# Optimization experiments

Measured on AMD Instinct MI355X. Metric: run time of the kernel, lower is better.

## Reference

```python
import jax, jax.numpy as jnp
import numpy as np

TAU_M = 20.0
DT = 1.0
V_TH = 1.0
V_RESET = 0.0
ALPHA = float(np.exp(-DT / TAU_M))  # membrane decay per step

B, T, I, H, O = 64, 1024, 128, 512, 10


def spike_fn(v):
    # Heaviside spike; surrogate grad handled in fwdbwd module.
    return (v >= 0.0).astype(v.dtype)


def setup_inputs() -> dict:
    key = jax.random.key(0)
    k = jax.random.split(key, 6)
    x = jax.random.normal(k[0], (B, T, I), dtype=jnp.float32)
    # input_projection: Linear(I, H) -> weight [H, I], bias [H]
    Wi = jax.random.normal(k[1], (H, I), dtype=jnp.float32) * (1.0 / np.sqrt(I))
    bi = jnp.zeros((H,), dtype=jnp.float32)
    # recurrent weight [H, H] (xavier-ish)
    Wr = jax.random.normal(k[2], (H, H), dtype=jnp.float32) * float(np.sqrt(2.0 / (H + H)))
    # readout: Linear(H, O)
    Wo = jax.random.normal(k[3], (O, H), dtype=jnp.float32) * (1.0 / np.sqrt(H))
    bo = jnp.zeros((O,), dtype=jnp.float32)
    return {"x": x, "Wi": Wi, "bi": bi, "Wr": Wr, "Wo": Wo, "bo": bo}


def reference(x, Wi, bi, Wr, Wo, bo):
    # Precompute input projection for all timesteps: [B, T, H]
    x_proj = jnp.einsum('bti,hi->bth', x, Wi) + bi

    def step(carry, cur_t):
        h, spikes_prev = carry
        total_current = cur_t + spikes_prev @ Wr        # [B, H]
        h = ALPHA * h + total_current                    # LIF leak + integrate
        spikes = spike_fn(h - V_TH)                      # threshold
        h = spikes * V_RESET + (1.0 - spikes) * h        # reset on spike
        return (h, spikes), spikes

    h0 = jnp.zeros((x.shape[0], Wr.shape[0]), dtype=x.dtype)
    s0 = jnp.zeros_like(h0)
    (_, _), hidden_states = jax.lax.scan(step, (h0, s0), jnp.swapaxes(x_proj, 0, 1))
    hidden_states = jnp.swapaxes(hidden_states, 0, 1)    # [B, T, H]

    hidden_mean = hidden_states.mean(axis=1)             # rate readout
    output = hidden_mean @ Wo.T + bo                     # [B, O]
    return output, hidden_states
```

## Files before the change

### kernel.cpp

```cpp
#include <hip/hip_runtime.h>


#define ALPHA_F 0.951229424500714f

typedef unsigned int u32x4 __attribute__((ext_vector_type(4)));

__device__ float g_mean[64 * 512];

__global__ __launch_bounds__(256) void xproj_kernel(
    const float* __restrict__ x, const float* __restrict__ Wi,
    const float* __restrict__ bi, float* __restrict__ out)
{
    __shared__ float xs[64][132];
    __shared__ float ws[32][132];

    const int tid = threadIdx.x;
    const int bm = blockIdx.x;
    const int bn = blockIdx.y;

    const float* xb = x  + (size_t)bm * 64 * 128;
    const float* wb = Wi + (size_t)bn * 32 * 128;

    for (int l = 0; l < 8; ++l) {
        int idx = l * 256 + tid;
        int row = idx >> 5, c4 = idx & 31;
        *(float4*)(&xs[row][c4 * 4]) = *(const float4*)(xb + row * 128 + c4 * 4);
    }
    for (int l = 0; l < 4; ++l) {
        int idx = l * 256 + tid;
        int row = idx >> 5, c4 = idx & 31;
        *(float4*)(&ws[row][c4 * 4]) = *(const float4*)(wb + row * 128 + c4 * 4);
    }
    __syncthreads();

    const int txh = tid & 15, txm = tid >> 4;
    const int m0 = txm * 4, h0 = txh * 2;

    float4 acc[4][2];
    #pragma unroll
    for (int mm = 0; mm < 4; ++mm)
        #pragma unroll
        for (int q = 0; q < 2; ++q)
            acc[mm][q] = make_float4(0.f, 0.f, 0.f, 0.f);

    for (int k4 = 0; k4 < 32; ++k4) {
        float4 a[4], b[2];
        #pragma unroll
        for (int mm = 0; mm < 4; ++mm) a[mm] = *(const float4*)(&xs[m0 + mm][k4 * 4]);
        #pragma unroll
        for (int q = 0; q < 2; ++q)    b[q]  = *(const float4*)(&ws[h0 + q][k4 * 4]);
        #pragma unroll
        for (int mm = 0; mm < 4; ++mm) {
            #pragma unroll
            for (int q = 0; q < 2; ++q) {
                float p0 = a[mm].x * b[q].x;
                float p1 = a[mm].y * b[q].y;
                float p2 = a[mm].z * b[q].z;
                float p3 = a[mm].w * b[q].w;
                asm volatile("" : "+v"(p0), "+v"(p1), "+v"(p2), "+v"(p3));
                acc[mm][q].x += p0;
                acc[mm][q].y += p1;
                acc[mm][q].z += p2;
                acc[mm][q].w += p3;
            }
        }
    }

    const int hbase = bn * 32 + h0;
    #pragma unroll
    for (int mm = 0; mm < 4; ++mm) {
        size_t m = (size_t)bm * 64 + m0 + mm;
        float2 o;
        {
            float s01 = acc[mm][0].x + acc[mm][0].y;
            float s23 = acc[mm][0].z + acc[mm][0].w;
            float hs  = s01 + s23;
            o.x = hs + bi[hbase + 0];
        }
        {
            float s01 = acc[mm][1].x + acc[mm][1].y;
            float s23 = acc[mm][1].z + acc[mm][1].w;
            float hs  = s01 + s23;
            o.y = hs + bi[hbase + 1];
        }
        *(float2*)(&out[m * 512 + hbase]) = o;
    }
}

struct C8 { float a, b, c, d, e, f, g, h; };

__device__ __forceinline__ C8 fetch8_lds(const unsigned short* lst, int cidx,
                                         const float (*wrs)[64], int lane) {
    uint4 L = ((const uint4*)lst)[cidx];
    int j0 = (int)(L.x & 0xffffu), j1 = (int)(L.x >> 16);
    int j2 = (int)(L.y & 0xffffu), j3 = (int)(L.y >> 16);
    int j4 = (int)(L.z & 0xffffu), j5 = (int)(L.z >> 16);
    int j6 = (int)(L.w & 0xffffu), j7 = (int)(L.w >> 16);
    C8 r;
    r.a = wrs[j0][lane]; r.b = wrs[j1][lane];
    r.c = wrs[j2][lane]; r.d = wrs[j3][lane];
    r.e = wrs[j4][lane]; r.f = wrs[j5][lane];
    r.g = wrs[j6][lane]; r.h = wrs[j7][lane];
    return r;
}

__device__ __forceinline__ void consume8(const C8& v, int e, int kA, int k,
                                         float& recA, float& recB) {
    if (e + 8 <= kA) {
        recA += v.a; recA += v.b; recA += v.c; recA += v.d;
        recA += v.e; recA += v.f; recA += v.g; recA += v.h;
    } else if (e >= kA && e + 8 <= k) {
        recB += v.a; recB += v.b; recB += v.c; recB += v.d;
        recB += v.e; recB += v.f; recB += v.g; recB += v.h;
    } else {
        if (e + 0 < k) { if (e + 0 < kA) recA += v.a; else recB += v.a; }
        if (e + 1 < k) { if (e + 1 < kA) recA += v.b; else recB += v.b; }
        if (e + 2 < k) { if (e + 2 < kA) recA += v.c; else recB += v.c; }
        if (e + 3 < k) { if (e + 3 < kA) recA += v.d; else recB += v.d; }
        if (e + 4 < k) { if (e + 4 < kA) recA += v.e; else recB += v.e; }
        if (e + 5 < k) { if (e + 5 < kA) recA += v.f; else recB += v.f; }
        if (e + 6 < k) { if (e + 6 < kA) recA += v.g; else recB += v.g; }
        if (e + 7 < k) { if (e + 7 < kA) recA += v.h; else recB += v.h; }
    }
}

__global__ __launch_bounds__(128, 1) void scan_kernel(
    const float* __restrict__ Wr, float* __restrict__ hid,
    u32x4* __restrict__ syn)
{
    const int blk  = blockIdx.x;
    const int p    = blk & 31;
    const int c    = blk >> 5;
    const int tid  = threadIdx.x;
    const int w    = tid >> 6;
    const int lane = tid & 63;
    const int s    = p + 32 * w;
    const int n    = (c << 6) + lane;

    __shared__ float wrs[512][64];
    __shared__ alignas(16) unsigned short lists[2][512];

    #pragma unroll
    for (int i = 0; i < 8; ++i) ((unsigned short*)lists)[tid * 8 + i] = 0;

    {
        const float* src = Wr + (c << 6);
        for (int it = 0; it < 64; ++it) {
            int idx = it * 128 + tid;
            int r = idx >> 4, q = idx & 15;
            float4 v = *(const float4*)(src + (size_t)r * 512 + q * 4);
            *(float4*)(&wrs[r][q * 4]) = v;
        }
    }
    __syncthreads();

    unsigned short* list = lists[w];
    float* base = hid + ((size_t)s * 1024) * 512 + n;

    float hstate = 0.0f;
    int cnt = 0;
    float xp = base[0];

    u32x4 prb0 = {0, 0, 0, 0}, prb1 = {0, 0, 0, 0};

    for (int t = 0; t < 1024; ++t) {
        int k = 0, kA = 0;
        if (t > 0) {
            const u32x4* pp = syn + ((((t - 1) & 1) * 64 + s) * 8) + (lane & 7);
            asm volatile("s_waitcnt vmcnt(0)" ::: "memory");
            u32x4 pv;
            asm volatile("global_load_dwordx4 %0, %2, off sc0 sc1\n\t"
                         "global_load_dwordx4 %1, %2, off sc0 sc1"
                         : "+v"(prb0), "+v"(prb1) : "v"(pp) : "memory");
            for (;;) {
                asm volatile("s_waitcnt vmcnt(1)" : "+v"(prb0) :: "memory");
                unsigned long long ok = __ballot(prb0.z == (unsigned)t);
                if ((ok & 0xFFull) == 0xFFull) { pv = prb0; break; }
                asm volatile("global_load_dwordx4 %0, %1, off sc0 sc1"
                             : "+v"(prb0) : "v"(pp) : "memory");
                asm volatile("s_waitcnt vmcnt(1)" : "+v"(prb1) :: "memory");
                ok = __ballot(prb1.z == (unsigned)t);
                if ((ok & 0xFFull) == 0xFFull) { pv = prb1; break; }
                asm volatile("global_load_dwordx4 %0, %1, off sc0 sc1"
                             : "+v"(prb1) : "v"(pp) : "memory");
            }
            unsigned long long fullm = (((unsigned long long)pv.y) << 32) | pv.x;
            int pc = __popcll(fullm);
            int sc_ = pc, u_;
            u_ = __shfl_up(sc_, 1); if (lane >= 1) sc_ += u_;
            u_ = __shfl_up(sc_, 2); if (lane >= 2) sc_ += u_;
            u_ = __shfl_up(sc_, 4); if (lane >= 4) sc_ += u_;
            int excl = sc_ - pc;
            k  = __builtin_amdgcn_readfirstlane(__shfl(sc_, 7));
            kA = __builtin_amdgcn_readfirstlane(__shfl(sc_, 5));
            unsigned mlo = (unsigned)__shfl((int)pv.x, lane >> 3);
            unsigned mhi = (unsigned)__shfl((int)pv.y, lane >> 3);
            int ep = __shfl(excl, lane >> 3);
            int sb = (lane & 7) * 8;
            unsigned byte; int below;
            if (sb < 32) {
                byte  = (mlo >> sb) & 0xFFu;
                below = __popc(mlo & ((1u << sb) - 1u));
            } else {
                byte  = (mhi >> (sb - 32)) & 0xFFu;
                below = __popc(mlo) + __popc(mhi & ((1u << (sb - 32)) - 1u));
            }
            int pos = ep + below;
            while (byte) {
                int bt = __builtin_ctz(byte);
                byte &= byte - 1;
                list[pos++] = (unsigned short)(lane * 8 + bt);
            }
        }

        float xp_next = base[(size_t)(t < 1023 ? t + 1 : 1023) * 512];

        float recA = 0.0f, recB = 0.0f;
        if (k > 0) {
            int nch = (k + 7) >> 3;
            C8 b0, b1;
            b0 = fetch8_lds(list, 0, wrs, lane);
            if (nch > 1) b1 = fetch8_lds(list, 1, wrs, lane);
            int cc = 0;
            for (; cc + 4 <= nch; cc += 2) {
                consume8(b0, (cc + 0) * 8, kA, k, recA, recB);
                b0 = fetch8_lds(list, cc + 2, wrs, lane);
                consume8(b1, (cc + 1) * 8, kA, k, recA, recB);
                b1 = fetch8_lds(list, cc + 3, wrs, lane);
            }
            int rem = nch - cc;
            if (rem >= 1) consume8(b0, (cc + 0) * 8, kA, k, recA, recB);
            if (rem >= 3) b0 = fetch8_lds(list, cc + 2, wrs, lane);
            if (rem >= 2) consume8(b1, (cc + 1) * 8, kA, k, recA, recB);
            if (rem >= 3) consume8(b0, (cc + 2) * 8, kA, k, recA, recB);
        }

        float rec = recA + recB;
        float cur = xp + rec;
        float tmp = ALPHA_F * hstate;
        asm volatile("" : "+v"(tmp));
        float hn = tmp + cur;
        bool sp = (hn >= 1.0f);
        hstate = sp ? 0.0f : hn;

        unsigned long long bm = __ballot(sp);
        if (lane == 0) {
            u32x4 pk;
            pk.x = (unsigned)bm; pk.y = (unsigned)(bm >> 32);
            pk.z = (unsigned)(t + 1); pk.w = 0u;
            u32x4* qp = syn + (((t & 1) * 64 + s) * 8) + c;
            asm volatile("global_store_dwordx4 %0, %1, off sc0 sc1"
                         :: "v"(qp), "v"(pk) : "memory");
        }

        base[(size_t)t * 512] = sp ? 1.0f : 0.0f;
        cnt += sp ? 1 : 0;
        xp = xp_next;
    }

    asm volatile("s_waitcnt vmcnt(0)" ::: "memory");
    asm volatile("" :: "v"(prb0), "v"(prb1));

    g_mean[s * 512 + n] = (float)cnt * (1.0f / 1024.0f);
}

__global__ __launch_bounds__(64) void readout_kernel(
    const float* __restrict__ Wo, const float* __restrict__ bo,
    float* __restrict__ out)
{
    const int b = blockIdx.x, o = blockIdx.y;
    const int lane = threadIdx.x;
    const float* mr = g_mean + b * 512;
    const float* wr = Wo + o * 512;
    double s = 0.0;
    for (int i = lane; i < 512; i += 64) s += (double)mr[i] * (double)wr[i];
    #pragma unroll
    for (int off = 32; off; off >>= 1) s += __shfl_down(s, off);
    if (lane == 0) out[b * 10 + o] = (float)(s + (double)bo[o]);
}

extern "C" void kernel_launch(void* const* d_in, const int* in_sizes, int n_in,
                              void* d_out, int out_size, void* d_ws, size_t ws_size,
                              hipStream_t stream) {
    const float* x  = (const float*)d_in[0];
    const float* Wi = (const float*)d_in[1];
    const float* bi = (const float*)d_in[2];
    const float* Wr = (const float*)d_in[3];
    const float* Wo = (const float*)d_in[4];
    const float* bo = (const float*)d_in[5];

    float* out = (float*)d_out;
    float* hid = out + 640;

    (void)hipMemsetAsync(d_ws, 0, 2 * 64 * 8 * 16, stream);

    dim3 gA(1024, 16);
    xproj_kernel<<<gA, 256, 0, stream>>>(x, Wi, bi, hid);

    scan_kernel<<<256, 128, 0, stream>>>(Wr, hid, (u32x4*)d_ws);

    dim3 gC(64, 10);
    readout_kernel<<<gC, 64, 0, stream>>>(Wo, bo, out);
}
```

Measured before the change: 2.084 ms.

## Store byte offsets in spike list and stage masks through LDS for prefix sums

```diff
diff --git a/kernel.cpp b/kernel.cpp
--- a/kernel.cpp
+++ b/kernel.cpp
@@ -89,18 +89,19 @@
 
 struct C8 { float a, b, c, d, e, f, g, h; };
 
-__device__ __forceinline__ C8 fetch8_lds(const unsigned short* lst, int cidx,
-                                         const float (*wrs)[64], int lane) {
-    uint4 L = ((const uint4*)lst)[cidx];
-    int j0 = (int)(L.x & 0xffffu), j1 = (int)(L.x >> 16);
-    int j2 = (int)(L.y & 0xffffu), j3 = (int)(L.y >> 16);
-    int j4 = (int)(L.z & 0xffffu), j5 = (int)(L.z >> 16);
-    int j6 = (int)(L.w & 0xffffu), j7 = (int)(L.w >> 16);
+__device__ __forceinline__ C8 fetch8v(const unsigned int* lst, int cidx,
+                                      const char* wbase, int lane4) {
+    u32x4 L0 = *(const u32x4*)(lst + cidx * 8);
+    u32x4 L1 = *(const u32x4*)(lst + cidx * 8 + 4);
     C8 r;
-    r.a = wrs[j0][lane]; r.b = wrs[j1][lane];
-    r.c = wrs[j2][lane]; r.d = wrs[j3][lane];
-    r.e = wrs[j4][lane]; r.f = wrs[j5][lane];
-    r.g = wrs[j6][lane]; r.h = wrs[j7][lane];
+    r.a = *(const float*)(wbase + (L0.x + lane4));
+    r.b = *(const float*)(wbase + (L0.y + lane4));
+    r.c = *(const float*)(wbase + (L0.z + lane4));
+    r.d = *(const float*)(wbase + (L0.w + lane4));
+    r.e = *(const float*)(wbase + (L1.x + lane4));
+    r.f = *(const float*)(wbase + (L1.y + lane4));
+    r.g = *(const float*)(wbase + (L1.z + lane4));
+    r.h = *(const float*)(wbase + (L1.w + lane4));
     return r;
 }
 
@@ -136,12 +137,14 @@
     const int lane = tid & 63;
     const int s    = p + 32 * w;
     const int n    = (c << 6) + lane;
+    const int lane4 = lane << 2;
 
     __shared__ float wrs[512][64];
-    __shared__ alignas(16) unsigned short lists[2][512];
+    __shared__ alignas(16) unsigned int lists[2][512];
+    __shared__ alignas(16) unsigned int maskbuf[2][16];
 
     #pragma unroll
-    for (int i = 0; i < 8; ++i) ((unsigned short*)lists)[tid * 8 + i] = 0;
+    for (int i = 0; i < 8; ++i) ((unsigned int*)lists)[i * 128 + tid] = 0;
 
     {
         const float* src = Wr + (c << 6);
@@ -154,7 +157,8 @@
     }
     __syncthreads();
 
-    unsigned short* list = lists[w];
+    unsigned int* list = lists[w];
+    const char* wbase = (const char*)&wrs[0][0];
     float* base = hid + ((size_t)s * 1024) * 512 + n;
 
     float hstate = 0.0f;
@@ -166,7 +170,7 @@
     for (int t = 0; t < 1024; ++t) {
         int k = 0, kA = 0;
         if (t > 0) {
-            const u32x4* pp = syn + ((((t - 1) & 1) * 64 + s) * 8) + (lane & 7);
+            const u32x4* pp = syn + ((((t - 1) & 1) * 64 + s) * 8) + (lane >> 3);
             asm volatile("s_waitcnt vmcnt(0)" ::: "memory");
             u32x4 pv;
             asm volatile("global_load_dwordx4 %0, %2, off sc0 sc1\n\t"
@@ -175,64 +179,82 @@
             for (;;) {
                 asm volatile("s_waitcnt vmcnt(1)" : "+v"(prb0) :: "memory");
                 unsigned long long ok = __ballot(prb0.z == (unsigned)t);
-                if ((ok & 0xFFull) == 0xFFull) { pv = prb0; break; }
+                if (ok == ~0ull) { pv = prb0; break; }
                 asm volatile("global_load_dwordx4 %0, %1, off sc0 sc1"
                              : "+v"(prb0) : "v"(pp) : "memory");
                 asm volatile("s_waitcnt vmcnt(1)" : "+v"(prb1) :: "memory");
                 ok = __ballot(prb1.z == (unsigned)t);
-                if ((ok & 0xFFull) == 0xFFull) { pv = prb1; break; }
+                if (ok == ~0ull) { pv = prb1; break; }
                 asm volatile("global_load_dwordx4 %0, %1, off sc0 sc1"
                              : "+v"(prb1) : "v"(pp) : "memory");
             }
-            unsigned long long fullm = (((unsigned long long)pv.y) << 32) | pv.x;
-            int pc = __popcll(fullm);
-            int sc_ = pc, u_;
-            u_ = __shfl_up(sc_, 1); if (lane >= 1) sc_ += u_;
-            u_ = __shfl_up(sc_, 2); if (lane >= 2) sc_ += u_;
-            u_ = __shfl_up(sc_, 4); if (lane >= 4) sc_ += u_;
-            int excl = sc_ - pc;
-            k  = __builtin_amdgcn_readfirstlane(__shfl(sc_, 7));
-            kA = __builtin_amdgcn_readfirstlane(__shfl(sc_, 5));
-            unsigned mlo = (unsigned)__shfl((int)pv.x, lane >> 3);
-            unsigned mhi = (unsigned)__shfl((int)pv.y, lane >> 3);
-            int ep = __shfl(excl, lane >> 3);
-            int sb = (lane & 7) * 8;
-            unsigned byte; int below;
-            if (sb < 32) {
-                byte  = (mlo >> sb) & 0xFFu;
-                below = __popc(mlo & ((1u << sb) - 1u));
-            } else {
-                byte  = (mhi >> (sb - 32)) & 0xFFu;
-                below = __popc(mlo) + __popc(mhi & ((1u << (sb - 32)) - 1u));
-            }
-            int pos = ep + below;
+
+            if ((lane & 7) == 0) {
+                unsigned long long mword =
+                    (((unsigned long long)pv.y) << 32) | (unsigned long long)pv.x;
+                *(unsigned long long*)&maskbuf[w][(lane >> 3) * 2] = mword;
+            }
+            u32x4 r0 = *(const u32x4*)&maskbuf[w][0];
+            u32x4 r1 = *(const u32x4*)&maskbuf[w][4];
+            u32x4 r2 = *(const u32x4*)&maskbuf[w][8];
+            u32x4 r3 = *(const u32x4*)&maskbuf[w][12];
+
+            int p0 = __popc(r0.x), p1 = __popc(r0.y), p2 = __popc(r0.z), p3 = __popc(r0.w);
+            int p4 = __popc(r1.x), p5 = __popc(r1.y), p6 = __popc(r1.z), p7 = __popc(r1.w);
+            int p8 = __popc(r2.x), p9 = __popc(r2.y), p10 = __popc(r2.z), p11 = __popc(r2.w);
+            int p12 = __popc(r3.x), p13 = __popc(r3.y), p14 = __popc(r3.z), p15 = __popc(r3.w);
+            int ka_ = p0 + p1 + p2 + p3 + p4 + p5 + p6 + p7 + p8 + p9 + p10 + p11;
+            int k_  = ka_ + p12 + p13 + p14 + p15;
+            kA = __builtin_amdgcn_readfirstlane(ka_);
+            k  = __builtin_amdgcn_readfirstlane(k_);
+
+            const int myW = lane >> 2;
+            int pre = 0;
+            if (myW >  0) pre += p0;   if (myW >  1) pre += p1;
+            if (myW >  2) pre += p2;   if (myW >  3) pre += p3;
+            if (myW >  4) pre += p4;   if (myW >  5) pre += p5;
+            if (myW >  6) pre += p6;   if (myW >  7) pre += p7;
+            if (myW >  8) pre += p8;   if (myW >  9) pre += p9;
+            if (myW > 10) pre += p10;  if (myW > 11) pre += p11;
+            if (myW > 12) pre += p12;  if (myW > 13) pre += p13;
+            if (myW > 14) pre += p14;
+            unsigned word = (lane & 4) ? pv.y : pv.x;
+            int shb = (lane & 3) * 8;
+            pre += __popc(word & ((1u << shb) - 1u));
+            unsigned byte = (word >> shb) & 0xFFu;
+
+            int pos = pre;
+            unsigned jbase = (unsigned)lane << 11;
             while (byte) {
                 int bt = __builtin_ctz(byte);
-                byte &= byte - 1;
-                list[pos++] = (unsigned short)(lane * 8 + bt);
+                byte &= byte - 1u;
+                list[pos++] = jbase + ((unsigned)bt << 8);
             }
         }
 
         float xp_next = base[(size_t)(t < 1023 ? t + 1 : 1023) * 512];
 
         float recA = 0.0f, recB = 0.0f;
-        if (k > 0) {
+        {
             int nch = (k + 7) >> 3;
-            C8 b0, b1;
-            b0 = fetch8_lds(list, 0, wrs, lane);
-            if (nch > 1) b1 = fetch8_lds(list, 1, wrs, lane);
+            C8 b0, b1, b2;
+            if (nch > 0) b0 = fetch8v(list, 0, wbase, lane4);
+            if (nch > 1) b1 = fetch8v(list, 1, wbase, lane4);
+            if (nch > 2) b2 = fetch8v(list, 2, wbase, lane4);
             int cc = 0;
-            for (; cc + 4 <= nch; cc += 2) {
-                consume8(b0, (cc + 0) * 8, kA, k, recA, recB);
-                b0 = fetch8_lds(list, cc + 2, wrs, lane);
-                consume8(b1, (cc + 1) * 8, kA, k, recA, recB);
-                b1 = fetch8_lds(list, cc + 3, wrs, lane);
+            for (; cc + 6 <= nch; cc += 3) {
+                consume8(b0, (cc + 0) * 8, kA, k, recA, recB); b0 = fetch8v(list, cc + 3, wbase, lane4);
+                consume8(b1, (cc + 1) * 8, kA, k, recA, recB); b1 = fetch8v(list, cc + 4, wbase, lane4);
+                consume8(b2, (cc + 2) * 8, kA, k, recA, recB); b2 = fetch8v(list, cc + 5, wbase, lane4);
             }
             int rem = nch - cc;
             if (rem >= 1) consume8(b0, (cc + 0) * 8, kA, k, recA, recB);
-            if (rem >= 3) b0 = fetch8_lds(list, cc + 2, wrs, lane);
+            if (rem >= 4) b0 = fetch8v(list, cc + 3, wbase, lane4);
             if (rem >= 2) consume8(b1, (cc + 1) * 8, kA, k, recA, recB);
-            if (rem >= 3) consume8(b0, (cc + 2) * 8, kA, k, recA, recB);
+            if (rem >= 5) b1 = fetch8v(list, cc + 4, wbase, lane4);
+            if (rem >= 3) consume8(b2, (cc + 2) * 8, kA, k, recA, recB);
+            if (rem >= 4) consume8(b0, (cc + 3) * 8, kA, k, recA, recB);
+            if (rem >= 5) consume8(b1, (cc + 4) * 8, kA, k, recA, recB);
         }
 
         float rec = recA + recB;
```

Result: no change. 2.100 ms (+0.8%).
